# Kernel tuning notes

Measured on AMD Instinct MI355X. Metric: run time of the kernel, lower is better.

## Reference

```python
import jax, jax.numpy as jnp
import numpy as np

N_NODES = 100000
N_EDGES = 3200000
IN_FEATS = 256
N_HIDDEN = 256
N_CLASSES = 40


def setup_inputs() -> dict:
    key = jax.random.key(0)
    ks = jax.random.split(key, 8)
    features = jax.random.normal(ks[0], (N_NODES, IN_FEATS), dtype=jnp.float32)
    src = jax.random.randint(ks[1], (N_EDGES,), 0, N_NODES, dtype=jnp.int64)
    dst = jax.random.randint(ks[2], (N_EDGES,), 0, N_NODES, dtype=jnp.int64)
    # Glorot-ish init scaled down for stability
    W0 = jax.random.normal(ks[3], (IN_FEATS, N_HIDDEN), dtype=jnp.float32) * (1.0 / np.sqrt(IN_FEATS))
    W1 = jax.random.normal(ks[4], (N_HIDDEN, N_HIDDEN), dtype=jnp.float32) * (1.0 / np.sqrt(N_HIDDEN))
    W2 = jax.random.normal(ks[5], (N_HIDDEN, N_CLASSES), dtype=jnp.float32) * (1.0 / np.sqrt(N_HIDDEN))
    b0 = jnp.zeros((N_HIDDEN,), jnp.float32)
    b1 = jnp.zeros((N_HIDDEN,), jnp.float32)
    b2 = jnp.zeros((N_CLASSES,), jnp.float32)
    return {"features": features, "src": src, "dst": dst,
            "W0": W0, "b0": b0, "W1": W1, "b1": b1, "W2": W2, "b2": b2}


def _degree_norms(src, dst, n_nodes):
    ones = jnp.ones(src.shape[0], jnp.float32)
    deg_out = jax.ops.segment_sum(ones, src, num_segments=n_nodes)
    deg_in = jax.ops.segment_sum(ones, dst, num_segments=n_nodes)
    # DGL norm='both': clamp degree to >=1 before rsqrt
    norm_out = jax.lax.rsqrt(jnp.maximum(deg_out, 1.0))  # applied on source side
    norm_in = jax.lax.rsqrt(jnp.maximum(deg_in, 1.0))    # applied on dest side
    return norm_out, norm_in


def _graph_conv(h, src, dst, norm_out, norm_in, W, b, activation):
    # h: [N, Fin]. norm='both': D_in^{-1/2} * A * (D_out^{-1/2} * h) @ W + b
    in_f, out_f = W.shape
    h = h * norm_out[:, None]
    if in_f > out_f:
        # mult weight first to reduce message width (DGL optimization, same math)
        h = h @ W
        agg = jax.ops.segment_sum(h[src], dst, num_segments=h.shape[0])
    else:
        agg = jax.ops.segment_sum(h[src], dst, num_segments=h.shape[0])
        agg = agg @ W
    out = agg * norm_in[:, None] + b
    if activation is not None:
        out = activation(out)
    return out


def reference(features, src, dst, W0, b0, W1, b1, W2, b2):
    n = features.shape[0]
    norm_out, norm_in = _degree_norms(src, dst, n)
    h = _graph_conv(features, src, dst, norm_out, norm_in, W0, b0, jax.nn.relu)
    h = _graph_conv(h, src, dst, norm_out, norm_in, W1, b1, jax.nn.relu)
    h = _graph_conv(h, src, dst, norm_out, norm_in, W2, b2, None)
    return h
```

## Files before the change

kernel.cpp:

```cpp
#include <hip/hip_runtime.h>

#define NN 100000
#define NE 3200000
#define F 256
#define NCLS 40
#define NC 391
#define NBLK_H 256
#define EPB (NE / NBLK_H)
#define CW 25000

using h4 = __attribute__((ext_vector_type(4))) _Float16;
using h8 = __attribute__((ext_vector_type(8))) _Float16;
using f4 = __attribute__((ext_vector_type(4))) float;

__global__ __launch_bounds__(256) void hist_k(const int* __restrict__ src,
                                              const int* __restrict__ dst,
                                              unsigned* __restrict__ pcnt,
                                              unsigned* __restrict__ pcc) {
    __shared__ unsigned hsrc[CW];
    __shared__ unsigned hc[NC];
    int t = threadIdx.x, b = blockIdx.x;
    for (int i = t; i < CW; i += 256) hsrc[i] = 0;
    for (int i = t; i < NC; i += 256) hc[i] = 0;
    __syncthreads();
    int beg = b * EPB, end = beg + EPB;
    for (int e = beg + t; e < end; e += 256) {
        int s = src[e];
        atomicAdd(&hsrc[s >> 2], 1u << (8 * (s & 3)));
        atomicAdd(&hc[dst[e] >> 8], 1u);
    }
    __syncthreads();
    unsigned* pc = pcnt + (size_t)b * CW;
    for (int i = t; i < CW; i += 256) pc[i] = hsrc[i];
    unsigned* pb = pcc + (size_t)b * NC;
    for (int i = t; i < NC; i += 256) pb[i] = hc[i];
}

__global__ __launch_bounds__(256) void redA_k(const unsigned* __restrict__ pcnt,
                                              unsigned* __restrict__ cntlo,
                                              unsigned* __restrict__ cnthi) {
    int w = blockIdx.x * 256 + threadIdx.x;
    if (w >= CW) return;
    int g = blockIdx.y;
    unsigned lo = 0, hi = 0;
    for (int b = g * 32; b < g * 32 + 32; b++) {
        unsigned v = pcnt[(size_t)b * CW + w];
        lo += (v & 255u) | (((v >> 8) & 255u) << 16);
        hi += ((v >> 16) & 255u) | ((v >> 24) << 16);
    }
    atomicAdd(&cntlo[w], lo);
    atomicAdd(&cnthi[w], hi);
}

__global__ void nout2_k(const unsigned* __restrict__ cntlo,
                        const unsigned* __restrict__ cnthi,
                        float* __restrict__ nout) {
    int w = blockIdx.x * blockDim.x + threadIdx.x;
    if (w >= CW) return;
    unsigned lo = cntlo[w], hi = cnthi[w];
    float4 o;
    o.x = rsqrtf(fmaxf((float)(lo & 0xFFFFu), 1.f));
    o.y = rsqrtf(fmaxf((float)(lo >> 16), 1.f));
    o.z = rsqrtf(fmaxf((float)(hi & 0xFFFFu), 1.f));
    o.w = rsqrtf(fmaxf((float)(hi >> 16), 1.f));
    *(float4*)(nout + w * 4) = o;
}

__global__ __launch_bounds__(256) void offsets_k(const unsigned* __restrict__ pcc,
                                                 unsigned* __restrict__ curoff,
                                                 unsigned* __restrict__ totals) {
    __shared__ unsigned sh[256];
    int c = blockIdx.x, t = threadIdx.x;
    unsigned v = pcc[(size_t)t * NC + c];
    sh[t] = v;
    __syncthreads();
    for (int off = 1; off < 256; off <<= 1) {
        unsigned x = (t >= off) ? sh[t - off] : 0;
        __syncthreads();
        sh[t] += x;
        __syncthreads();
    }
    curoff[(size_t)t * NC + c] = sh[t] - v;
    if (t == 255) totals[c] = sh[255];
}

__global__ __launch_bounds__(512) void base_k(const unsigned* __restrict__ totals,
                                              int* __restrict__ cbase) {
    __shared__ unsigned sh[512];
    int t = threadIdx.x;
    unsigned v = (t < NC) ? totals[t] : 0;
    sh[t] = v;
    __syncthreads();
    for (int off = 1; off < 512; off <<= 1) {
        unsigned x = (t >= off) ? sh[t - off] : 0;
        __syncthreads();
        sh[t] += x;
        __syncthreads();
    }
    if (t < NC) cbase[t] = (int)(sh[t] - v);
    if (t == 0) cbase[NC] = NE;
}

__global__ __launch_bounds__(256) void p1scat_k(const int* __restrict__ src,
                                                const int* __restrict__ dst,
                                                const int* __restrict__ cbase,
                                                const unsigned* __restrict__ curoff,
                                                unsigned* __restrict__ ebuf) {
    __shared__ int cur[NC];
    int t = threadIdx.x, b = blockIdx.x;
    for (int i = t; i < NC; i += 256)
        cur[i] = cbase[i] + (int)curoff[(size_t)b * NC + i];
    __syncthreads();
    int beg = b * EPB, end = beg + EPB;
    for (int e = beg + t; e < end; e += 256) {
        int d = dst[e];
        int p = atomicAdd(&cur[d >> 8], 1);
        ebuf[p] = (unsigned)src[e] | ((unsigned)(d & 255) << 17);
    }
}

__global__ __launch_bounds__(256) void p2build_k(const int* __restrict__ cbase,
                                                 const unsigned* __restrict__ ebuf,
                                                 int* __restrict__ csr_src,
                                                 int* __restrict__ row_ptr,
                                                 float* __restrict__ nin) {
    __shared__ int cnt[256], cur[256], sh[256];
    int c = blockIdx.x, t = threadIdx.x;
    int beg = cbase[c], end = cbase[c + 1];
    cnt[t] = 0;
    __syncthreads();
    for (int e = beg + t; e < end; e += 256)
        atomicAdd(&cnt[(ebuf[e] >> 17) & 255], 1);
    __syncthreads();
    int v = cnt[t];
    sh[t] = v;
    __syncthreads();
    for (int off = 1; off < 256; off <<= 1) {
        int x = (t >= off) ? sh[t - off] : 0;
        __syncthreads();
        sh[t] += x;
        __syncthreads();
    }
    int pref = sh[t] - v;
    int node = c * 256 + t;
    if (node <= NN) row_ptr[node] = beg + pref;
    if (node < NN)  nin[node] = rsqrtf(fmaxf((float)v, 1.f));
    cur[t] = pref;
    __syncthreads();
    for (int e = beg + t; e < end; e += 256) {
        unsigned w = ebuf[e];
        int p = atomicAdd(&cur[(w >> 17) & 255], 1);
        csr_src[beg + p] = (int)(w & 0x1FFFFu);
    }
}

__global__ void convfeat_k(const float4* __restrict__ fin, const float* __restrict__ nout,
                           h4* __restrict__ fout, int n4) {
    int i = blockIdx.x * blockDim.x + threadIdx.x;
    if (i < n4) {
        float s = nout[i >> 6];
        float4 v = fin[i];
        h4 o;
        o[0] = (_Float16)(v.x * s);
        o[1] = (_Float16)(v.y * s);
        o[2] = (_Float16)(v.z * s);
        o[3] = (_Float16)(v.w * s);
        fout[i] = o;
    }
}

__global__ void convw_all_k(const float* __restrict__ W0, const float* __restrict__ W1,
                            const float* __restrict__ W2,
                            _Float16* __restrict__ Wt0, _Float16* __restrict__ Wt1,
                            _Float16* __restrict__ Wt2) {
    int i = blockIdx.x * blockDim.x + threadIdx.x;
    if (i < 65536) {
        int n = i >> 8, k = i & 255;
        Wt0[i] = (_Float16)W0[k * 256 + n];
    } else if (i < 131072) {
        int j = i - 65536;
        int n = j >> 8, k = j & 255;
        Wt1[j] = (_Float16)W1[k * 256 + n];
    } else if (i < 147456) {
        int j = i - 131072;
        int n = j >> 8, k = j & 255;
        Wt2[j] = (n < NCLS) ? (_Float16)W2[k * NCLS + n] : (_Float16)0.0f;
    }
}

__global__ __launch_bounds__(256) void agg256h_k(
        const int* __restrict__ row_ptr, const int* __restrict__ csr_src,
        const _Float16* __restrict__ h, _Float16* __restrict__ agg, int nN) {
    int node = (blockIdx.x * blockDim.x + threadIdx.x) >> 6;
    int lane = threadIdx.x & 63;
    if (node >= nN) return;
    int half = lane >> 5, col = lane & 31;
    int beg = row_ptr[node], end = row_ptr[node + 1];
    f4 a[4][2];
#pragma unroll
    for (int u = 0; u < 4; u++) { a[u][0] = (f4){0,0,0,0}; a[u][1] = (f4){0,0,0,0}; }
    int e = beg;
    for (; e + 7 < end; e += 8) {
        int s[4];
#pragma unroll
        for (int u = 0; u < 4; u++) s[u] = csr_src[e + 2 * u + half];
        h8 v[4];
#pragma unroll
        for (int u = 0; u < 4; u++)
            v[u] = *(const h8*)(h + (size_t)s[u] * F + col * 8);
#pragma unroll
        for (int u = 0; u < 4; u++)
#pragma unroll
            for (int j = 0; j < 8; j++) a[u][j >> 2][j & 3] += (float)v[u][j];
    }
    for (int t = e + half; t < end; t += 2) {
        h8 v = *(const h8*)(h + (size_t)csr_src[t] * F + col * 8);
#pragma unroll
        for (int j = 0; j < 8; j++) a[0][j >> 2][j & 3] += (float)v[j];
    }
    float r[8];
#pragma unroll
    for (int j = 0; j < 8; j++)
        r[j] = (a[0][j >> 2][j & 3] + a[1][j >> 2][j & 3])
             + (a[2][j >> 2][j & 3] + a[3][j >> 2][j & 3]);
#pragma unroll
    for (int j = 0; j < 8; j++) r[j] += __shfl_xor(r[j], 32);
    if (half == 0) {
        h8 o;
#pragma unroll
        for (int j = 0; j < 8; j++) o[j] = (_Float16)r[j];
        *(h8*)(agg + (size_t)node * F + col * 8) = o;
    }
}

__global__ __launch_bounds__(256) void agg64h_k(
        const int* __restrict__ row_ptr, const int* __restrict__ csr_src,
        const _Float16* __restrict__ t3, const float* __restrict__ nin,
        const float* __restrict__ b2, float* __restrict__ out, int nN) {
    int node = (blockIdx.x * blockDim.x + threadIdx.x) >> 6;
    int lane = threadIdx.x & 63;
    if (node >= nN) return;
    int q = lane >> 4, c = lane & 15;
    int beg = row_ptr[node], end = row_ptr[node + 1];
    f4 a0 = {0,0,0,0}, a1 = {0,0,0,0};
    int e = beg;
    for (; e + 7 < end; e += 8) {
        int s0 = csr_src[e + q], s1 = csr_src[e + 4 + q];
        h4 v0 = *(const h4*)(t3 + (size_t)s0 * 64 + c * 4);
        h4 v1 = *(const h4*)(t3 + (size_t)s1 * 64 + c * 4);
#pragma unroll
        for (int j = 0; j < 4; j++) { a0[j] += (float)v0[j]; a1[j] += (float)v1[j]; }
    }
    for (int t = e + q; t < end; t += 4) {
        h4 v = *(const h4*)(t3 + (size_t)csr_src[t] * 64 + c * 4);
#pragma unroll
        for (int j = 0; j < 4; j++) a0[j] += (float)v[j];
    }
    float r[4];
#pragma unroll
    for (int j = 0; j < 4; j++) {
        r[j] = a0[j] + a1[j];
        r[j] += __shfl_xor(r[j], 16);
        r[j] += __shfl_xor(r[j], 32);
    }
    if (lane < 10) {
        float ni = nin[node];
        float4 o;
        o.x = r[0] * ni + b2[lane * 4 + 0];
        o.y = r[1] * ni + b2[lane * 4 + 1];
        o.z = r[2] * ni + b2[lane * 4 + 2];
        o.w = r[3] * ni + b2[lane * 4 + 3];
        *(float4*)(out + (size_t)node * NCLS + lane * 4) = o;
    }
}

template <int NT, int EPI>
__global__ __launch_bounds__(1024) void gemm_lds_k(
        const _Float16* __restrict__ A, const _Float16* __restrict__ Wt,
        _Float16* __restrict__ C, int M,
        const float* __restrict__ nin, const float* __restrict__ nout,
        const float* __restrict__ bias) {
    constexpr int COLS = NT * 16;
    __shared__ _Float16 lds[COLS * 256];
    char* ldsb = (char*)lds;

    const int tid  = threadIdx.x;
    const int lane = tid & 63;
    const int w    = tid >> 6;
    const int row0 = blockIdx.x * 256;

#pragma unroll
    for (int i = 0; i < COLS / 32; i++) {
        int idx  = (i * 1024 + tid) * 8;
        int byte = idx * 2;
        int row  = byte >> 9;
        int swz  = byte ^ ((row & 7) << 4);
        *(h8*)(ldsb + swz) = *(const h8*)(Wt + idx);
    }

    int arow = row0 + w * 16 + (lane & 15);
    if (arow >= M) arow = M - 1;
    const _Float16* Ap = A + (size_t)arow * 256 + (lane >> 4) * 8;
    h8 areg[8];
#pragma unroll
    for (int i = 0; i < 8; i++) areg[i] = *(const h8*)(Ap + i * 32);

    __syncthreads();

    f4 acc[NT];
#pragma unroll
    for (int n = 0; n < NT; n++) acc[n] = (f4){0.f, 0.f, 0.f, 0.f};

#pragma unroll
    for (int k0 = 0; k0 < 8; k0++) {
        int kb = (k0 * 32 + (lane >> 4) * 8) * 2;
#pragma unroll
        for (int n = 0; n < NT; n++) {
            int r    = n * 16 + (lane & 15);
            int byte = r * 512 + kb;
            int swz  = byte ^ ((r & 7) << 4);
            h8 bf = *(const h8*)(ldsb + swz);
            acc[n] = __builtin_amdgcn_mfma_f32_16x16x32_f16(areg[k0], bf, acc[n], 0, 0, 0);
        }
    }

    __syncthreads();

    const int g  = lane >> 4;
    const int rb = row0 + w * 16 + g * 4;
    float si[4], so[4];
    if (EPI) {
#pragma unroll
        for (int r = 0; r < 4; r++) {
            int rr = rb + r; if (rr >= M) rr = M - 1;
            si[r] = nin[rr];
            so[r] = nout[rr];
        }
    }
    char* warea = ldsb + w * (16 * COLS * 2);
#pragma unroll
    for (int n = 0; n < NT; n++) {
        float bb = EPI ? bias[n * 16 + (lane & 15)] : 0.f;
#pragma unroll
        for (int r = 0; r < 4; r++) {
            float x = acc[n][r];
            if (EPI) x = fmaxf(x * si[r] + bb, 0.f) * so[r];
            int lrow = g * 4 + r;
            int lcol = n * 16 + (lane & 15);
            *(_Float16*)(warea + (size_t)(lrow * COLS + lcol) * 2) = (_Float16)x;
        }
    }

    _Float16* Crow = C + (size_t)(row0 + w * 16) * COLS;
#pragma unroll
    for (int i = 0; i < COLS / 32; i++) {
        int off  = i * 1024 + lane * 16;
        int lrow = off / (COLS * 2);
        int grow = row0 + w * 16 + lrow;
        h8 v = *(const h8*)(warea + off);
        if (grow < M) *(h8*)((char*)Crow + off) = v;
    }
}

extern "C" void kernel_launch(void* const* d_in, const int* in_sizes, int n_in,
                              void* d_out, int out_size, void* d_ws, size_t ws_size,
                              hipStream_t stream) {
    const float* features = (const float*)d_in[0];
    const int*   src      = (const int*)d_in[1];
    const int*   dst      = (const int*)d_in[2];
    const float* W0       = (const float*)d_in[3];
    const float* b0       = (const float*)d_in[4];
    const float* W1       = (const float*)d_in[5];
    const float* b1       = (const float*)d_in[6];
    const float* W2       = (const float*)d_in[7];
    const float* b2       = (const float*)d_in[8];
    float* out = (float*)d_out;

    char* ws = (char*)d_ws;
    const size_t H_BYTES = (size_t)NN * F * 2;
    _Float16* hA   = (_Float16*)(ws);
    _Float16* hB   = (_Float16*)(ws + H_BYTES);
    _Float16* t3h  = (_Float16*)(ws + 2 * H_BYTES);
    char* q = ws + 2 * H_BYTES + (size_t)NN * 64 * 2;
    int* csr_src    = (int*)q;               q += (size_t)NE * 4;
    unsigned* ebuf  = (unsigned*)q;          q += (size_t)NE * 4;
    unsigned* pcnt  = (unsigned*)q;          q += (size_t)NBLK_H * CW * 4;
    unsigned* pcc   = (unsigned*)q;          q += (size_t)NBLK_H * NC * 4 + 1024;
    unsigned* curoff= (unsigned*)q;          q += (size_t)NBLK_H * NC * 4 + 1024;
    char* p = q;
    const size_t SB = 401408;
    unsigned* totals = (unsigned*)(p + 0 * SB);
    int*   cbase   = (int*)(p + 1 * SB);
    int*   row_ptr = (int*)(p + 2 * SB);
    float* nout    = (float*)(p + 3 * SB);
    float* nin     = (float*)(p + 4 * SB);
    unsigned* cntlo = (unsigned*)(p + 5 * SB);
    unsigned* cnthi = (unsigned*)(p + 6 * SB);
    _Float16* Wt0  = (_Float16*)(p + 7 * SB);
    _Float16* Wt1  = (_Float16*)(p + 7 * SB + 131072);
    _Float16* Wt2  = (_Float16*)(p + 7 * SB + 262144);

    const int AGG_BLOCKS = (NN * 64 + 255) / 256;
    const int GB = (NN + 255) / 256;

    hipMemsetAsync(cntlo, 0, CW * 4, stream);
    hipMemsetAsync(cnthi, 0, CW * 4, stream);
    hist_k<<<NBLK_H, 256, 0, stream>>>(src, dst, pcnt, pcc);
    {
        dim3 rg((CW + 255) / 256, 8);
        redA_k<<<rg, 256, 0, stream>>>(pcnt, cntlo, cnthi);
    }
    nout2_k<<<(CW + 255) / 256, 256, 0, stream>>>(cntlo, cnthi, nout);
    offsets_k<<<NC, 256, 0, stream>>>(pcc, curoff, totals);
    base_k<<<1, 512, 0, stream>>>(totals, cbase);
    p1scat_k<<<NBLK_H, 256, 0, stream>>>(src, dst, cbase, curoff, ebuf);
    p2build_k<<<NC, 256, 0, stream>>>(cbase, ebuf, csr_src, row_ptr, nin);

    int n4 = NN * 64;
    convfeat_k<<<(n4 + 255) / 256, 256, 0, stream>>>((const float4*)features, nout,
                                                     (h4*)hB, n4);
    convw_all_k<<<576, 256, 0, stream>>>(W0, W1, W2, Wt0, Wt1, Wt2);

    agg256h_k<<<AGG_BLOCKS, 256, 0, stream>>>(row_ptr, csr_src, hB, hA, NN);
    gemm_lds_k<16, 1><<<GB, 1024, 0, stream>>>(hA, Wt0, hB, NN, nin, nout, b0);

    agg256h_k<<<AGG_BLOCKS, 256, 0, stream>>>(row_ptr, csr_src, hB, hA, NN);
    gemm_lds_k<16, 1><<<GB, 1024, 0, stream>>>(hA, Wt1, hB, NN, nin, nout, b1);

    gemm_lds_k<4, 0><<<GB, 1024, 0, stream>>>(hB, Wt2, t3h, NN, nullptr, nullptr, nullptr);
    agg64h_k<<<AGG_BLOCKS, 256, 0, stream>>>(row_ptr, csr_src, t3h, nin, b2, out, NN);
}
```

Measured before the change: 898.8 us.

## Widen CSR-build blocks, fuse feature/weight conversion, vectorize final aggregation

Raises the thread count of the histogram, scatter and CSR-build kernels from 256 to 512 so more edges are processed concurrently per block. Merges the feature conversion and weight transposition into a single launch to save one kernel launch. Reworks the final 40-class aggregation so each lane loads 8 halves instead of 4 and processes 16 edges per iteration, with an extra shuffle stage in the reduction. It also writes row_ptr[NN] explicitly, and more threads per block means more LDS atomic contention in the build kernels.

Result: faster. 840.7 us (-6.5%).

```diff
diff --git a/kernel.cpp b/kernel.cpp
--- a/kernel.cpp
+++ b/kernel.cpp
@@ -13,27 +13,27 @@
 using h8 = __attribute__((ext_vector_type(8))) _Float16;
 using f4 = __attribute__((ext_vector_type(4))) float;
 
-__global__ __launch_bounds__(256) void hist_k(const int* __restrict__ src,
+__global__ __launch_bounds__(512) void hist_k(const int* __restrict__ src,
                                               const int* __restrict__ dst,
                                               unsigned* __restrict__ pcnt,
                                               unsigned* __restrict__ pcc) {
     __shared__ unsigned hsrc[CW];
     __shared__ unsigned hc[NC];
     int t = threadIdx.x, b = blockIdx.x;
-    for (int i = t; i < CW; i += 256) hsrc[i] = 0;
-    for (int i = t; i < NC; i += 256) hc[i] = 0;
+    for (int i = t; i < CW; i += 512) hsrc[i] = 0;
+    for (int i = t; i < NC; i += 512) hc[i] = 0;
     __syncthreads();
     int beg = b * EPB, end = beg + EPB;
-    for (int e = beg + t; e < end; e += 256) {
+    for (int e = beg + t; e < end; e += 512) {
         int s = src[e];
         atomicAdd(&hsrc[s >> 2], 1u << (8 * (s & 3)));
         atomicAdd(&hc[dst[e] >> 8], 1u);
     }
     __syncthreads();
     unsigned* pc = pcnt + (size_t)b * CW;
-    for (int i = t; i < CW; i += 256) pc[i] = hsrc[i];
+    for (int i = t; i < CW; i += 512) pc[i] = hsrc[i];
     unsigned* pb = pcc + (size_t)b * NC;
-    for (int i = t; i < NC; i += 256) pb[i] = hc[i];
+    for (int i = t; i < NC; i += 512) pb[i] = hc[i];
 }
 
 __global__ __launch_bounds__(256) void redA_k(const unsigned* __restrict__ pcnt,
@@ -101,25 +101,25 @@
     if (t == 0) cbase[NC] = NE;
 }
 
-__global__ __launch_bounds__(256) void p1scat_k(const int* __restrict__ src,
+__global__ __launch_bounds__(512) void p1scat_k(const int* __restrict__ src,
                                                 const int* __restrict__ dst,
                                                 const int* __restrict__ cbase,
                                                 const unsigned* __restrict__ curoff,
                                                 unsigned* __restrict__ ebuf) {
     __shared__ int cur[NC];
     int t = threadIdx.x, b = blockIdx.x;
-    for (int i = t; i < NC; i += 256)
+    for (int i = t; i < NC; i += 512)
         cur[i] = cbase[i] + (int)curoff[(size_t)b * NC + i];
     __syncthreads();
     int beg = b * EPB, end = beg + EPB;
-    for (int e = beg + t; e < end; e += 256) {
+    for (int e = beg + t; e < end; e += 512) {
         int d = dst[e];
         int p = atomicAdd(&cur[d >> 8], 1);
         ebuf[p] = (unsigned)src[e] | ((unsigned)(d & 255) << 17);
     }
 }
 
-__global__ __launch_bounds__(256) void p2build_k(const int* __restrict__ cbase,
+__global__ __launch_bounds__(512) void p2build_k(const int* __restrict__ cbase,
                                                  const unsigned* __restrict__ ebuf,
                                                  int* __restrict__ csr_src,
                                                  int* __restrict__ row_ptr,
@@ -127,37 +127,45 @@
     __shared__ int cnt[256], cur[256], sh[256];
     int c = blockIdx.x, t = threadIdx.x;
     int beg = cbase[c], end = cbase[c + 1];
-    cnt[t] = 0;
-    __syncthreads();
-    for (int e = beg + t; e < end; e += 256)
+    if (t < 256) cnt[t] = 0;
+    __syncthreads();
+    for (int e = beg + t; e < end; e += 512)
         atomicAdd(&cnt[(ebuf[e] >> 17) & 255], 1);
     __syncthreads();
-    int v = cnt[t];
-    sh[t] = v;
+    int v = 0;
+    if (t < 256) { v = cnt[t]; sh[t] = v; }
     __syncthreads();
     for (int off = 1; off < 256; off <<= 1) {
-        int x = (t >= off) ? sh[t - off] : 0;
-        __syncthreads();
-        sh[t] += x;
-        __syncthreads();
-    }
-    int pref = sh[t] - v;
-    int node = c * 256 + t;
-    if (node <= NN) row_ptr[node] = beg + pref;
-    if (node < NN)  nin[node] = rsqrtf(fmaxf((float)v, 1.f));
-    cur[t] = pref;
-    __syncthreads();
-    for (int e = beg + t; e < end; e += 256) {
+        int x = (t < 256 && t >= off) ? sh[t - off] : 0;
+        __syncthreads();
+        if (t < 256) sh[t] += x;
+        __syncthreads();
+    }
+    if (t < 256) {
+        int pref = sh[t] - v;
+        int node = c * 256 + t;
+        if (node <= NN) row_ptr[node] = beg + pref;
+        if (node < NN)  nin[node] = rsqrtf(fmaxf((float)v, 1.f));
+        cur[t] = pref;
+    }
+    if (c == 0 && t == 0) row_ptr[NN] = NE;
+    __syncthreads();
+    for (int e = beg + t; e < end; e += 512) {
         unsigned w = ebuf[e];
         int p = atomicAdd(&cur[(w >> 17) & 255], 1);
         csr_src[beg + p] = (int)(w & 0x1FFFFu);
     }
 }
 
-__global__ void convfeat_k(const float4* __restrict__ fin, const float* __restrict__ nout,
-                           h4* __restrict__ fout, int n4) {
+__global__ void conv_fused_k(const float4* __restrict__ fin, const float* __restrict__ nout,
+                             h4* __restrict__ fout,
+                             const float* __restrict__ W0, const float* __restrict__ W1,
+                             const float* __restrict__ W2,
+                             _Float16* __restrict__ Wt0, _Float16* __restrict__ Wt1,
+                             _Float16* __restrict__ Wt2) {
     int i = blockIdx.x * blockDim.x + threadIdx.x;
-    if (i < n4) {
+    const int N4 = NN * 64;
+    if (i < N4) {
         float s = nout[i >> 6];
         float4 v = fin[i];
         h4 o;
@@ -166,25 +174,20 @@
         o[2] = (_Float16)(v.z * s);
         o[3] = (_Float16)(v.w * s);
         fout[i] = o;
-    }
-}
-
-__global__ void convw_all_k(const float* __restrict__ W0, const float* __restrict__ W1,
-                            const float* __restrict__ W2,
-                            _Float16* __restrict__ Wt0, _Float16* __restrict__ Wt1,
-                            _Float16* __restrict__ Wt2) {
-    int i = blockIdx.x * blockDim.x + threadIdx.x;
-    if (i < 65536) {
-        int n = i >> 8, k = i & 255;
-        Wt0[i] = (_Float16)W0[k * 256 + n];
-    } else if (i < 131072) {
-        int j = i - 65536;
-        int n = j >> 8, k = j & 255;
-        Wt1[j] = (_Float16)W1[k * 256 + n];
-    } else if (i < 147456) {
-        int j = i - 131072;
-        int n = j >> 8, k = j & 255;
-        Wt2[j] = (n < NCLS) ? (_Float16)W2[k * NCLS + n] : (_Float16)0.0f;
+    } else {
+        int j = i - N4;
+        if (j < 65536) {
+            int n = j >> 8, k = j & 255;
+            Wt0[j] = (_Float16)W0[k * 256 + n];
+        } else if (j < 131072) {
+            int jj = j - 65536;
+            int n = jj >> 8, k = jj & 255;
+            Wt1[jj] = (_Float16)W1[k * 256 + n];
+        } else if (j < 147456) {
+            int jj = j - 131072;
+            int n = jj >> 8, k = jj & 255;
+            Wt2[jj] = (n < NCLS) ? (_Float16)W2[k * NCLS + n] : (_Float16)0.0f;
+        }
     }
 }
 
@@ -240,37 +243,45 @@
     int node = (blockIdx.x * blockDim.x + threadIdx.x) >> 6;
     int lane = threadIdx.x & 63;
     if (node >= nN) return;
-    int q = lane >> 4, c = lane & 15;
+    int grp = lane >> 3, c = lane & 7;
     int beg = row_ptr[node], end = row_ptr[node + 1];
-    f4 a0 = {0,0,0,0}, a1 = {0,0,0,0};
+    float a0[8], a1[8];
+#pragma unroll
+    for (int j = 0; j < 8; j++) { a0[j] = 0.f; a1[j] = 0.f; }
     int e = beg;
-    for (; e + 7 < end; e += 8) {
-        int s0 = csr_src[e + q], s1 = csr_src[e + 4 + q];
-        h4 v0 = *(const h4*)(t3 + (size_t)s0 * 64 + c * 4);
-        h4 v1 = *(const h4*)(t3 + (size_t)s1 * 64 + c * 4);
-#pragma unroll
-        for (int j = 0; j < 4; j++) { a0[j] += (float)v0[j]; a1[j] += (float)v1[j]; }
-    }
-    for (int t = e + q; t < end; t += 4) {
-        h4 v = *(const h4*)(t3 + (size_t)csr_src[t] * 64 + c * 4);
-#pragma unroll
-        for (int j = 0; j < 4; j++) a0[j] += (float)v[j];
-    }
-    float r[4];
-#pragma unroll
-    for (int j = 0; j < 4; j++) {
+    for (; e + 15 < end; e += 16) {
+        int s0 = csr_src[e + grp], s1 = csr_src[e + 8 + grp];
+        h8 v0 = *(const h8*)(t3 + (size_t)s0 * 64 + c * 8);
+        h8 v1 = *(const h8*)(t3 + (size_t)s1 * 64 + c * 8);
+#pragma unroll
+        for (int j = 0; j < 8; j++) { a0[j] += (float)v0[j]; a1[j] += (float)v1[j]; }
+    }
+    for (int t = e + grp; t < end; t += 8) {
+        h8 v = *(const h8*)(t3 + (size_t)csr_src[t] * 64 + c * 8);
+#pragma unroll
+        for (int j = 0; j < 8; j++) a0[j] += (float)v[j];
+    }
+    float r[8];
+#pragma unroll
+    for (int j = 0; j < 8; j++) {
         r[j] = a0[j] + a1[j];
+        r[j] += __shfl_xor(r[j], 8);
         r[j] += __shfl_xor(r[j], 16);
         r[j] += __shfl_xor(r[j], 32);
     }
-    if (lane < 10) {
+    if (grp == 0 && c < 5) {
         float ni = nin[node];
         float4 o;
-        o.x = r[0] * ni + b2[lane * 4 + 0];
-        o.y = r[1] * ni + b2[lane * 4 + 1];
-        o.z = r[2] * ni + b2[lane * 4 + 2];
-        o.w = r[3] * ni + b2[lane * 4 + 3];
-        *(float4*)(out + (size_t)node * NCLS + lane * 4) = o;
+        o.x = r[0] * ni + b2[c * 8 + 0];
+        o.y = r[1] * ni + b2[c * 8 + 1];
+        o.z = r[2] * ni + b2[c * 8 + 2];
+        o.w = r[3] * ni + b2[c * 8 + 3];
+        *(float4*)(out + (size_t)node * NCLS + c * 8) = o;
+        o.x = r[4] * ni + b2[c * 8 + 4];
+        o.y = r[5] * ni + b2[c * 8 + 5];
+        o.z = r[6] * ni + b2[c * 8 + 6];
+        o.w = r[7] * ni + b2[c * 8 + 7];
+        *(float4*)(out + (size_t)node * NCLS + c * 8 + 4) = o;
     }
 }
 
@@ -405,7 +416,7 @@
 
     hipMemsetAsync(cntlo, 0, CW * 4, stream);
     hipMemsetAsync(cnthi, 0, CW * 4, stream);
-    hist_k<<<NBLK_H, 256, 0, stream>>>(src, dst, pcnt, pcc);
+    hist_k<<<NBLK_H, 512, 0, stream>>>(src, dst, pcnt, pcc);
     {
         dim3 rg((CW + 255) / 256, 8);
         redA_k<<<rg, 256, 0, stream>>>(pcnt, cntlo, cnthi);
@@ -413,13 +424,14 @@
     nout2_k<<<(CW + 255) / 256, 256, 0, stream>>>(cntlo, cnthi, nout);
     offsets_k<<<NC, 256, 0, stream>>>(pcc, curoff, totals);
     base_k<<<1, 512, 0, stream>>>(totals, cbase);
-    p1scat_k<<<NBLK_H, 256, 0, stream>>>(src, dst, cbase, curoff, ebuf);
-    p2build_k<<<NC, 256, 0, stream>>>(cbase, ebuf, csr_src, row_ptr, nin);
-
-    int n4 = NN * 64;
-    convfeat_k<<<(n4 + 255) / 256, 256, 0, stream>>>((const float4*)features, nout,
-                                                     (h4*)hB, n4);
-    convw_all_k<<<576, 256, 0, stream>>>(W0, W1, W2, Wt0, Wt1, Wt2);
+    p1scat_k<<<NBLK_H, 512, 0, stream>>>(src, dst, cbase, curoff, ebuf);
+    p2build_k<<<NC, 512, 0, stream>>>(cbase, ebuf, csr_src, row_ptr, nin);
+
+    {
+        int total = NN * 64 + 147456;
+        conv_fused_k<<<(total + 255) / 256, 256, 0, stream>>>(
+            (const float4*)features, nout, (h4*)hB, W0, W1, W2, Wt0, Wt1, Wt2);
+    }
 
     agg256h_k<<<AGG_BLOCKS, 256, 0, stream>>>(row_ptr, csr_src, hB, hA, NN);
     gemm_lds_k<16, 1><<<GB, 1024, 0, stream>>>(hA, Wt0, hB, NN, nin, nout, b0);
```
